# Optimization experiments

Hardware: AMD Instinct MI355X
Metric: run time of the kernel (lower is better)

## Reference

```python
import math
import jax, jax.numpy as jnp
import numpy as np

HEADS = 9
EMBED = 32
TEMPERATURE = 3000.0

def _conv1x1(x, W, b):
    # x: [B,C,H,W], W: [O,C], b: [O]  (1x1 conv == channel matmul)
    return jnp.einsum('bchw,oc->bohw', x, W) + b[None, :, None, None]

def setup_inputs() -> dict:
    key = jax.random.key(0)
    ks = jax.random.split(key, 14)
    B, H, W = 2, 64, 64
    h2, w2 = 32, 32
    hd = HEADS * EMBED  # 288
    s = 0.1
    return {
        'second_frame': jax.random.normal(ks[0], (B, 3, H, W), jnp.float32),
        'first_frame_aligned': jax.random.normal(ks[1], (B, 3, H, W), jnp.float32),
        'second_frame_feat': jax.random.normal(ks[2], (B, 4, h2, w2), jnp.float32),
        'first_frame_feat_aligned': jax.random.normal(ks[3], (B, 4, h2, w2), jnp.float32),
        'Wq': jax.random.normal(ks[4], (hd, 3), jnp.float32) * s,
        'bq': jax.random.normal(ks[5], (hd,), jnp.float32) * s,
        'Wk': jax.random.normal(ks[6], (hd, 3), jnp.float32) * s,
        'bk': jax.random.normal(ks[7], (hd,), jnp.float32) * s,
        'Wv': jax.random.normal(ks[8], (hd, 4), jnp.float32) * s,
        'bv': jax.random.normal(ks[9], (hd,), jnp.float32) * s,
        'Wp': jax.random.normal(ks[10], (4, hd), jnp.float32) * s,
        'bp': jax.random.normal(ks[11], (4,), jnp.float32) * s,
        'Wt': jax.random.normal(ks[12], (1, EMBED), jnp.float32) * s,
        'bt': jax.random.normal(ks[13], (1,), jnp.float32) * s,
    }

def reference(second_frame, first_frame_aligned, second_frame_feat,
              first_frame_feat_aligned, Wq, bq, Wk, bk, Wv, bv, Wp, bp, Wt, bt):
    B, _, H, W = second_frame.shape
    HW = H * W
    # bilinear upsample of aligned features to (H, W); half-pixel centers == align_corners=False
    feat_up = jax.image.resize(first_frame_feat_aligned,
                               (B, first_frame_feat_aligned.shape[1], H, W),
                               method='linear', antialias=False)
    Q = _conv1x1(second_frame, Wq, bq).reshape(B, HEADS, EMBED, HW)
    K = _conv1x1(first_frame_aligned, Wk, bk).reshape(B, HEADS, EMBED, HW)
    V = _conv1x1(feat_up, Wv, bv).reshape(B, HEADS, EMBED, HW)
    Qn = jnp.transpose(Q, (0, 1, 3, 2))                      # [B,h,HW,d]
    sim = jnp.einsum('bhnd,bhdm->bhnm', Qn, K) / math.sqrt(EMBED)  # [B,h,HW,HW]
    # learned per-query threshold from Q
    t = jnp.einsum('bhnd,od->bhno', Qn, Wt) + bt             # [B,h,HW,1]
    attn = jax.nn.relu((sim - t) / TEMPERATURE)              # no row normalization
    out = jnp.einsum('bhnm,bhdm->bhnd', attn, V)             # [B,h,HW,d]
    out = jnp.transpose(out, (0, 1, 3, 2)).reshape(B, HEADS * EMBED, H, W)
    out_feat = _conv1x1(out, Wp, bp)                         # [B,4,H,W]
    h2, w2 = second_frame_feat.shape[-2:]
    out_feat_down = jax.image.resize(out_feat, (B, out_feat.shape[1], h2, w2),
                                     method='linear', antialias=False)
    final_feat = second_frame_feat + out_feat_down
    return final_feat, out_feat_down
```

## Files before the change

### kernel.cpp

```cpp
#include <hip/hip_runtime.h>
#include <hip/hip_bf16.h>
#include <cstddef>

#define NHEADS 9
#define D 32
#define SQ 4096
#define ZSPLIT 8
#define MBLK (SQ / ZSPLIT)
#define CHUNKS (MBLK / 64)
#define KROW 40
#define VROW 72

typedef __attribute__((ext_vector_type(8))) short bf16x8;
typedef __attribute__((ext_vector_type(4))) short bf16x4;
typedef __attribute__((ext_vector_type(4))) float f32x4;

__device__ __forceinline__ unsigned int f2bf(float f) {
    unsigned int u = __float_as_uint(f);
    u += 0x7fffu + ((u >> 16) & 1u);
    return u >> 16;
}

__device__ __forceinline__ unsigned int trunc_pk(float lo, float hi) {
    return __builtin_amdgcn_perm(__float_as_uint(hi), __float_as_uint(lo),
                                 0x07060302u);
}

__device__ __forceinline__ bf16x8 relu_pack8(f32x4 s1, f32x4 s2) {
    const f32x4 zz = {0.f, 0.f, 0.f, 0.f};
    f32x4 a = __builtin_elementwise_max(s1, zz);
    f32x4 b = __builtin_elementwise_max(s2, zz);
    union { unsigned int u[4]; bf16x8 v; } P;
    P.u[0] = trunc_pk(a[0], a[1]);
    P.u[1] = trunc_pk(a[2], a[3]);
    P.u[2] = trunc_pk(b[0], b[1]);
    P.u[3] = trunc_pk(b[2], b[3]);
    return P.v;
}

__global__ __launch_bounds__(256) void prep_kernel(
    const float* __restrict__ x2, const float* __restrict__ x1,
    const float* __restrict__ feat1,
    const float* __restrict__ Wq, const float* __restrict__ bq,
    const float* __restrict__ Wk, const float* __restrict__ bk,
    const float* __restrict__ Wv, const float* __restrict__ bv,
    const float* __restrict__ Wt, const float* __restrict__ bt,
    unsigned short* __restrict__ Qb, unsigned short* __restrict__ Kb,
    unsigned short* __restrict__ Vt, float* __restrict__ tbuf,
    float* __restrict__ of)
{
    int idx = blockIdx.x * blockDim.x + threadIdx.x;
    if (idx < 2 * 4 * SQ) of[idx] = 0.0f;
    int g  = idx & 3;
    int n  = (idx >> 2) & (SQ - 1);
    int bh = idx >> 14;
    int h  = bh % NHEADS;
    int b  = bh / NHEADS;

    float xs0 = x2[((size_t)b * 3 + 0) * SQ + n];
    float xs1 = x2[((size_t)b * 3 + 1) * SQ + n];
    float xs2 = x2[((size_t)b * 3 + 2) * SQ + n];
    float ys0 = x1[((size_t)b * 3 + 0) * SQ + n];
    float ys1 = x1[((size_t)b * 3 + 1) * SQ + n];
    float ys2 = x1[((size_t)b * 3 + 2) * SQ + n];

    int yy = n >> 6, xx = n & 63;
    int jy = yy >> 1, jx = xx >> 1;
    int j0, j1, i0, i1; float wy0, wy1, wx0, wx1;
    if (yy & 1) { j0 = jy; j1 = (jy < 31) ? jy + 1 : 31; wy0 = 0.75f; wy1 = 0.25f; }
    else        { j0 = (jy > 0) ? jy - 1 : 0; j1 = jy;   wy0 = 0.25f; wy1 = 0.75f; }
    if (xx & 1) { i0 = jx; i1 = (jx < 31) ? jx + 1 : 31; wx0 = 0.75f; wx1 = 0.25f; }
    else        { i0 = (jx > 0) ? jx - 1 : 0; i1 = jx;   wx0 = 0.25f; wx1 = 0.75f; }

    float fu[4];
#pragma unroll
    for (int c = 0; c < 4; ++c) {
        const float* f = feat1 + ((size_t)b * 4 + c) * 1024;
        fu[c] = wy0 * (wx0 * f[j0 * 32 + i0] + wx1 * f[j0 * 32 + i1]) +
                wy1 * (wx0 * f[j1 * 32 + i0] + wx1 * f[j1 * 32 + i1]);
    }

    const int d0 = g * 8;
    unsigned int qp[4], kp[4];
    float tpart = 0.0f;
#pragma unroll
    for (int j = 0; j < 8; ++j) {
        int d = d0 + j, hd = h * D + d;
        float q = bq[hd] + Wq[hd * 3] * xs0 + Wq[hd * 3 + 1] * xs1 + Wq[hd * 3 + 2] * xs2;
        float k = bk[hd] + Wk[hd * 3] * ys0 + Wk[hd * 3 + 1] * ys1 + Wk[hd * 3 + 2] * ys2;
        float v = bv[hd] + Wv[hd * 4] * fu[0] + Wv[hd * 4 + 1] * fu[1] +
                  Wv[hd * 4 + 2] * fu[2] + Wv[hd * 4 + 3] * fu[3];
        tpart += q * Wt[d];
        unsigned int qb_ = f2bf(q), kb_ = f2bf(k);
        if (j & 1) { qp[j >> 1] |= qb_ << 16; kp[j >> 1] |= kb_ << 16; }
        else       { qp[j >> 1]  = qb_;       kp[j >> 1]  = kb_; }
        Vt[((size_t)bh * D + d) * SQ + n] = (unsigned short)f2bf(v);
    }
    tpart += __shfl_xor(tpart, 1);
    tpart += __shfl_xor(tpart, 2);
    if (g == 0) tbuf[(size_t)bh * SQ + n] = tpart + bt[0];

    size_t base = ((size_t)bh * SQ + n) * D + d0;
    *(uint4*)(Qb + base) = make_uint4(qp[0], qp[1], qp[2], qp[3]);
    *(uint4*)(Kb + base) = make_uint4(kp[0], kp[1], kp[2], kp[3]);
}

__global__ __launch_bounds__(256, 4) void attn_kernel(
    const unsigned short* __restrict__ Qb,
    const unsigned short* __restrict__ Kb,
    const unsigned short* __restrict__ Vt,
    const float* __restrict__ tbuf,
    const float* __restrict__ Wp,
    float* __restrict__ of)
{
    __shared__ __align__(16) unsigned short Ks[64 * KROW];
    __shared__ __align__(16) unsigned short Vs[32 * VROW];

    const int bh   = blockIdx.y;
    const int h    = bh % NHEADS;
    const int b    = bh / NHEADS;
    const int n0   = blockIdx.x * 256;
    const int mc0  = blockIdx.z * MBLK;
    const int tid  = threadIdx.x;
    const int wave = tid >> 6;
    const int lane = tid & 63;
    const int l15  = lane & 15;
    const int quad = lane >> 4;

    const int nw = n0 + wave * 64;

    const unsigned short* qbase = Qb + ((size_t)bh * SQ + nw + l15) * D + quad * 8;
    bf16x8 qfA = *(const bf16x8*)(qbase);
    bf16x8 qfB = *(const bf16x8*)(qbase + 16 * D);
    bf16x8 qfC = *(const bf16x8*)(qbase + 32 * D);
    bf16x8 qfD = *(const bf16x8*)(qbase + 48 * D);

    const float SQRT32 = 5.656854249492381f;
    const float* tb = tbuf + (size_t)bh * SQ + nw + l15;
    float TA = tb[0]  * SQRT32;
    float TB = tb[16] * SQRT32;
    float TC = tb[32] * SQRT32;
    float TD = tb[48] * SQRT32;
    const f32x4 ciA = {-TA, -TA, -TA, -TA};
    const f32x4 ciB = {-TB, -TB, -TB, -TB};
    const f32x4 ciC = {-TC, -TC, -TC, -TC};
    const f32x4 ciD = {-TD, -TD, -TD, -TD};

    const uint4* Kg4 = (const uint4*)(Kb + (size_t)bh * SQ * D);
    const uint4* Vg4 = (const uint4*)(Vt + (size_t)bh * D * SQ);

    const int krow = tid >> 2;
    const int kcol = (tid & 3) * 8;
    const int kslot = (krow & 32) + 4 * ((krow >> 3) & 3) + (krow & 3) + ((krow & 4) << 2);
    unsigned short* kdst = Ks + kslot * KROW + kcol;
    const int vd = tid >> 3;
    const int vm = (tid & 7) * 8;
    unsigned short* vdst = Vs + vd * VROW + vm;
    const int vgbase = vd * (SQ / 8) + (mc0 >> 3) + (tid & 7);

    f32x4 accAl = {0.f,0.f,0.f,0.f}, accAh = {0.f,0.f,0.f,0.f};
    f32x4 accBl = {0.f,0.f,0.f,0.f}, accBh = {0.f,0.f,0.f,0.f};
    f32x4 accCl = {0.f,0.f,0.f,0.f}, accCh = {0.f,0.f,0.f,0.f};
    f32x4 accDl = {0.f,0.f,0.f,0.f}, accDh = {0.f,0.f,0.f,0.f};

    uint4 kreg = Kg4[(size_t)mc0 * 4 + tid];
    uint4 vreg = Vg4[vgbase];

    for (int c = 0; c < CHUNKS; ++c) {
        __syncthreads();
        *(uint4*)kdst = kreg;
        *(uint4*)vdst = vreg;
        kreg = Kg4[(size_t)(mc0 + (c + 1) * 64) * 4 + tid];
        vreg = Vg4[vgbase + (c + 1) * 8];
        __syncthreads();

#pragma unroll
        for (int g32 = 0; g32 < 2; ++g32) {
            const unsigned short* kbase = Ks + g32 * 32 * KROW;
            bf16x8 kf1 = *(const bf16x8*)(kbase + l15 * KROW + quad * 8);
            bf16x8 kf2 = *(const bf16x8*)(kbase + (16 + l15) * KROW + quad * 8);
            bf16x8 vlo = *(const bf16x8*)(Vs + l15 * VROW + g32 * 32 + quad * 8);
            bf16x8 vhi = *(const bf16x8*)(Vs + (l15 + 16) * VROW + g32 * 32 + quad * 8);

            f32x4 sA1 = __builtin_amdgcn_mfma_f32_16x16x32_bf16(kf1, qfA, ciA, 0, 0, 0);
            f32x4 sA2 = __builtin_amdgcn_mfma_f32_16x16x32_bf16(kf2, qfA, ciA, 0, 0, 0);
            f32x4 sB1 = __builtin_amdgcn_mfma_f32_16x16x32_bf16(kf1, qfB, ciB, 0, 0, 0);
            f32x4 sB2 = __builtin_amdgcn_mfma_f32_16x16x32_bf16(kf2, qfB, ciB, 0, 0, 0);
            f32x4 sC1 = __builtin_amdgcn_mfma_f32_16x16x32_bf16(kf1, qfC, ciC, 0, 0, 0);
            f32x4 sC2 = __builtin_amdgcn_mfma_f32_16x16x32_bf16(kf2, qfC, ciC, 0, 0, 0);
            f32x4 sD1 = __builtin_amdgcn_mfma_f32_16x16x32_bf16(kf1, qfD, ciD, 0, 0, 0);
            f32x4 sD2 = __builtin_amdgcn_mfma_f32_16x16x32_bf16(kf2, qfD, ciD, 0, 0, 0);

            bf16x8 pA = relu_pack8(sA1, sA2);
            bf16x8 pB = relu_pack8(sB1, sB2);
            bf16x8 pC = relu_pack8(sC1, sC2);
            bf16x8 pD = relu_pack8(sD1, sD2);

            accAl = __builtin_amdgcn_mfma_f32_16x16x32_bf16(vlo, pA, accAl, 0, 0, 0);
            accAh = __builtin_amdgcn_mfma_f32_16x16x32_bf16(vhi, pA, accAh, 0, 0, 0);
            accBl = __builtin_amdgcn_mfma_f32_16x16x32_bf16(vlo, pB, accBl, 0, 0, 0);
            accBh = __builtin_amdgcn_mfma_f32_16x16x32_bf16(vhi, pB, accBh, 0, 0, 0);
            accCl = __builtin_amdgcn_mfma_f32_16x16x32_bf16(vlo, pC, accCl, 0, 0, 0);
            accCh = __builtin_amdgcn_mfma_f32_16x16x32_bf16(vhi, pC, accCh, 0, 0, 0);
            accDl = __builtin_amdgcn_mfma_f32_16x16x32_bf16(vlo, pD, accDl, 0, 0, 0);
            accDh = __builtin_amdgcn_mfma_f32_16x16x32_bf16(vhi, pD, accDh, 0, 0, 0);
        }
    }

    const float s1 = 5.892556509887896e-05f;
    const float* wph = Wp + h * D + quad * 4;
#pragma unroll
    for (int o = 0; o < 4; ++o) {
        float cA = 0.f, cB = 0.f, cC = 0.f, cD = 0.f;
#pragma unroll
        for (int r = 0; r < 4; ++r) {
            float wlo = wph[o * 288 + r], whi = wph[o * 288 + 16 + r];
            cA += accAl[r] * wlo + accAh[r] * whi;
            cB += accBl[r] * wlo + accBh[r] * whi;
            cC += accCl[r] * wlo + accCh[r] * whi;
            cD += accDl[r] * wlo + accDh[r] * whi;
        }
        cA += __shfl_xor(cA, 16); cA += __shfl_xor(cA, 32);
        cB += __shfl_xor(cB, 16); cB += __shfl_xor(cB, 32);
        cC += __shfl_xor(cC, 16); cC += __shfl_xor(cC, 32);
        cD += __shfl_xor(cD, 16); cD += __shfl_xor(cD, 32);
        if (quad == 0) {
            float* ob = &of[((size_t)b * 4 + o) * SQ + nw + l15];
            atomicAdd(ob,      cA * s1);
            atomicAdd(ob + 16, cB * s1);
            atomicAdd(ob + 32, cC * s1);
            atomicAdd(ob + 48, cD * s1);
        }
    }
}

__global__ void final_kernel(const float* __restrict__ of,
                             const float* __restrict__ sff,
                             const float* __restrict__ bp,
                             float* __restrict__ dout)
{
    int tid = blockIdx.x * blockDim.x + threadIdx.x;
    if (tid >= 8192) return;
    int i  = tid & 31;
    int jj = (tid >> 5) & 31;
    int bo = tid >> 10;
    int o  = bo & 3;
    const float* src = of + (size_t)bo * SQ;
    int y = jj * 2, x = i * 2;
    float dval = 0.25f * (src[y * 64 + x] + src[y * 64 + x + 1] +
                          src[(y + 1) * 64 + x] + src[(y + 1) * 64 + x + 1]) + bp[o];
    dout[tid]        = sff[tid] + dval;
    dout[8192 + tid] = dval;
}

extern "C" void kernel_launch(void* const* d_in, const int* in_sizes, int n_in,
                              void* d_out, int out_size, void* d_ws, size_t ws_size,
                              hipStream_t stream)
{
    const float* second_frame = (const float*)d_in[0];
    const float* first_frame  = (const float*)d_in[1];
    const float* sff          = (const float*)d_in[2];
    const float* ffa          = (const float*)d_in[3];
    const float* Wq = (const float*)d_in[4];
    const float* bq = (const float*)d_in[5];
    const float* Wk = (const float*)d_in[6];
    const float* bk = (const float*)d_in[7];
    const float* Wv = (const float*)d_in[8];
    const float* bv = (const float*)d_in[9];
    const float* Wp = (const float*)d_in[10];
    const float* bp = (const float*)d_in[11];
    const float* Wt = (const float*)d_in[12];
    const float* bt = (const float*)d_in[13];
    float* out = (float*)d_out;

    char* ws = (char*)d_ws;
    const size_t QKV = (size_t)2 * NHEADS * SQ * D * sizeof(unsigned short);
    unsigned short* Qb = (unsigned short*)ws;
    unsigned short* Kb = (unsigned short*)(ws + QKV);
    unsigned short* Vt = (unsigned short*)(ws + 2 * QKV);
    float* tbuf = (float*)(ws + 3 * QKV);
    float* of   = (float*)(ws + 3 * QKV + (size_t)2 * NHEADS * SQ * sizeof(float));

    prep_kernel<<<1152, 256, 0, stream>>>(second_frame, first_frame, ffa,
                                          Wq, bq, Wk, bk, Wv, bv, Wt, bt,
                                          Qb, Kb, Vt, tbuf, of);
    dim3 ag(16, 18, ZSPLIT);
    attn_kernel<<<ag, 256, 0, stream>>>(Qb, Kb, Vt, tbuf, Wp, of);
    final_kernel<<<32, 256, 0, stream>>>(of, sff, bp, out);
}
```

Baseline: 138.2 us.

## Double-buffer K/V in LDS and coalesce V transpose store via shared memory

The attention loop now uses two LDS buffers for K and V, storing the next chunk while computing the current one. This halves the barriers per chunk and uses a custom barrier that waits only on LDS counters, not on outstanding global loads. The prep kernel stages V through shared memory so the transposed V writes become coalesced 8-byte stores instead of scattered 2-byte stores. The cost is more LDS per block, which may reduce occupancy, and the prefetch loads read past the block's chunk range on the last iterations.

```diff
diff --git a/kernel.cpp b/kernel.cpp
--- a/kernel.cpp
+++ b/kernel.cpp
@@ -19,6 +19,10 @@
     unsigned int u = __float_as_uint(f);
     u += 0x7fffu + ((u >> 16) & 1u);
     return u >> 16;
+}
+
+__device__ __forceinline__ void lds_barrier() {
+    asm volatile("s_waitcnt lgkmcnt(0)\n\ts_barrier" ::: "memory");
 }
 
 __device__ __forceinline__ unsigned int trunc_pk(float lo, float hi) {
@@ -49,9 +53,13 @@
     unsigned short* __restrict__ Vt, float* __restrict__ tbuf,
     float* __restrict__ of)
 {
-    int idx = blockIdx.x * blockDim.x + threadIdx.x;
+    __shared__ unsigned short Vls[32 * 66];
+
+    const int tid = threadIdx.x;
+    int idx = blockIdx.x * blockDim.x + tid;
     if (idx < 2 * 4 * SQ) of[idx] = 0.0f;
     int g  = idx & 3;
+    int nl = tid >> 2;
     int n  = (idx >> 2) & (SQ - 1);
     int bh = idx >> 14;
     int h  = bh % NHEADS;
@@ -94,7 +102,7 @@
         unsigned int qb_ = f2bf(q), kb_ = f2bf(k);
         if (j & 1) { qp[j >> 1] |= qb_ << 16; kp[j >> 1] |= kb_ << 16; }
         else       { qp[j >> 1]  = qb_;       kp[j >> 1]  = kb_; }
-        Vt[((size_t)bh * D + d) * SQ + n] = (unsigned short)f2bf(v);
+        Vls[d * 66 + nl] = (unsigned short)f2bf(v);
     }
     tpart += __shfl_xor(tpart, 1);
     tpart += __shfl_xor(tpart, 2);
@@ -103,7 +111,49 @@
     size_t base = ((size_t)bh * SQ + n) * D + d0;
     *(uint4*)(Qb + base) = make_uint4(qp[0], qp[1], qp[2], qp[3]);
     *(uint4*)(Kb + base) = make_uint4(kp[0], kp[1], kp[2], kp[3]);
-}
+
+    __syncthreads();
+    {
+        int r  = tid >> 3;
+        int c4 = tid & 7;
+        int n0 = (blockIdx.x & 63) * 64;
+        unsigned int w0 = *(const unsigned int*)&Vls[r * 66 + c4 * 4];
+        unsigned int w1 = *(const unsigned int*)&Vls[r * 66 + c4 * 4 + 2];
+        *(uint2*)(Vt + ((size_t)bh * D + r) * SQ + n0 + c4 * 4) = make_uint2(w0, w1);
+    }
+}
+
+#define COMPUTE(KS, VS)                                                          \
+    {                                                                            \
+        _Pragma("unroll")                                                        \
+        for (int g32 = 0; g32 < 2; ++g32) {                                      \
+            const unsigned short* kbase = KS + g32 * 32 * KROW;                  \
+            bf16x8 kf1 = *(const bf16x8*)(kbase + l15 * KROW + quad * 8);        \
+            bf16x8 kf2 = *(const bf16x8*)(kbase + (16 + l15) * KROW + quad * 8); \
+            bf16x8 vlo = *(const bf16x8*)(VS + l15 * VROW + g32 * 32 + quad * 8);\
+            bf16x8 vhi = *(const bf16x8*)(VS + (l15 + 16) * VROW + g32 * 32 + quad * 8);\
+            f32x4 sA1 = __builtin_amdgcn_mfma_f32_16x16x32_bf16(kf1, qfA, ciA, 0, 0, 0);\
+            f32x4 sA2 = __builtin_amdgcn_mfma_f32_16x16x32_bf16(kf2, qfA, ciA, 0, 0, 0);\
+            f32x4 sB1 = __builtin_amdgcn_mfma_f32_16x16x32_bf16(kf1, qfB, ciB, 0, 0, 0);\
+            f32x4 sB2 = __builtin_amdgcn_mfma_f32_16x16x32_bf16(kf2, qfB, ciB, 0, 0, 0);\
+            f32x4 sC1 = __builtin_amdgcn_mfma_f32_16x16x32_bf16(kf1, qfC, ciC, 0, 0, 0);\
+            f32x4 sC2 = __builtin_amdgcn_mfma_f32_16x16x32_bf16(kf2, qfC, ciC, 0, 0, 0);\
+            f32x4 sD1 = __builtin_amdgcn_mfma_f32_16x16x32_bf16(kf1, qfD, ciD, 0, 0, 0);\
+            f32x4 sD2 = __builtin_amdgcn_mfma_f32_16x16x32_bf16(kf2, qfD, ciD, 0, 0, 0);\
+            bf16x8 pA = relu_pack8(sA1, sA2);                                    \
+            bf16x8 pB = relu_pack8(sB1, sB2);                                    \
+            bf16x8 pC = relu_pack8(sC1, sC2);                                    \
+            bf16x8 pD = relu_pack8(sD1, sD2);                                    \
+            accAl = __builtin_amdgcn_mfma_f32_16x16x32_bf16(vlo, pA, accAl, 0, 0, 0);\
+            accAh = __builtin_amdgcn_mfma_f32_16x16x32_bf16(vhi, pA, accAh, 0, 0, 0);\
+            accBl = __builtin_amdgcn_mfma_f32_16x16x32_bf16(vlo, pB, accBl, 0, 0, 0);\
+            accBh = __builtin_amdgcn_mfma_f32_16x16x32_bf16(vhi, pB, accBh, 0, 0, 0);\
+            accCl = __builtin_amdgcn_mfma_f32_16x16x32_bf16(vlo, pC, accCl, 0, 0, 0);\
+            accCh = __builtin_amdgcn_mfma_f32_16x16x32_bf16(vhi, pC, accCh, 0, 0, 0);\
+            accDl = __builtin_amdgcn_mfma_f32_16x16x32_bf16(vlo, pD, accDl, 0, 0, 0);\
+            accDh = __builtin_amdgcn_mfma_f32_16x16x32_bf16(vhi, pD, accDh, 0, 0, 0);\
+        }                                                                        \
+    }
 
 __global__ __launch_bounds__(256, 4) void attn_kernel(
     const unsigned short* __restrict__ Qb,
@@ -113,8 +163,10 @@
     const float* __restrict__ Wp,
     float* __restrict__ of)
 {
-    __shared__ __align__(16) unsigned short Ks[64 * KROW];
-    __shared__ __align__(16) unsigned short Vs[32 * VROW];
+    __shared__ __align__(16) unsigned short Ks0[64 * KROW];
+    __shared__ __align__(16) unsigned short Ks1[64 * KROW];
+    __shared__ __align__(16) unsigned short Vs0[32 * VROW];
+    __shared__ __align__(16) unsigned short Vs1[32 * VROW];
 
     const int bh   = blockIdx.y;
     const int h    = bh % NHEADS;
@@ -152,10 +204,12 @@
     const int krow = tid >> 2;
     const int kcol = (tid & 3) * 8;
     const int kslot = (krow & 32) + 4 * ((krow >> 3) & 3) + (krow & 3) + ((krow & 4) << 2);
-    unsigned short* kdst = Ks + kslot * KROW + kcol;
+    unsigned short* kdst0 = Ks0 + kslot * KROW + kcol;
+    unsigned short* kdst1 = Ks1 + kslot * KROW + kcol;
     const int vd = tid >> 3;
     const int vm = (tid & 7) * 8;
-    unsigned short* vdst = Vs + vd * VROW + vm;
+    unsigned short* vdst0 = Vs0 + vd * VROW + vm;
+    unsigned short* vdst1 = Vs1 + vd * VROW + vm;
     const int vgbase = vd * (SQ / 8) + (mc0 >> 3) + (tid & 7);
 
     f32x4 accAl = {0.f,0.f,0.f,0.f}, accAh = {0.f,0.f,0.f,0.f};
@@ -163,48 +217,27 @@
     f32x4 accCl = {0.f,0.f,0.f,0.f}, accCh = {0.f,0.f,0.f,0.f};
     f32x4 accDl = {0.f,0.f,0.f,0.f}, accDh = {0.f,0.f,0.f,0.f};
 
-    uint4 kreg = Kg4[(size_t)mc0 * 4 + tid];
-    uint4 vreg = Vg4[vgbase];
-
-    for (int c = 0; c < CHUNKS; ++c) {
-        __syncthreads();
-        *(uint4*)kdst = kreg;
-        *(uint4*)vdst = vreg;
-        kreg = Kg4[(size_t)(mc0 + (c + 1) * 64) * 4 + tid];
-        vreg = Vg4[vgbase + (c + 1) * 8];
-        __syncthreads();
-
-#pragma unroll
-        for (int g32 = 0; g32 < 2; ++g32) {
-            const unsigned short* kbase = Ks + g32 * 32 * KROW;
-            bf16x8 kf1 = *(const bf16x8*)(kbase + l15 * KROW + quad * 8);
-            bf16x8 kf2 = *(const bf16x8*)(kbase + (16 + l15) * KROW + quad * 8);
-            bf16x8 vlo = *(const bf16x8*)(Vs + l15 * VROW + g32 * 32 + quad * 8);
-            bf16x8 vhi = *(const bf16x8*)(Vs + (l15 + 16) * VROW + g32 * 32 + quad * 8);
-
-            f32x4 sA1 = __builtin_amdgcn_mfma_f32_16x16x32_bf16(kf1, qfA, ciA, 0, 0, 0);
-            f32x4 sA2 = __builtin_amdgcn_mfma_f32_16x16x32_bf16(kf2, qfA, ciA, 0, 0, 0);
-            f32x4 sB1 = __builtin_amdgcn_mfma_f32_16x16x32_bf16(kf1, qfB, ciB, 0, 0, 0);
-            f32x4 sB2 = __builtin_amdgcn_mfma_f32_16x16x32_bf16(kf2, qfB, ciB, 0, 0, 0);
-            f32x4 sC1 = __builtin_amdgcn_mfma_f32_16x16x32_bf16(kf1, qfC, ciC, 0, 0, 0);
-            f32x4 sC2 = __builtin_amdgcn_mfma_f32_16x16x32_bf16(kf2, qfC, ciC, 0, 0, 0);
-            f32x4 sD1 = __builtin_amdgcn_mfma_f32_16x16x32_bf16(kf1, qfD, ciD, 0, 0, 0);
-            f32x4 sD2 = __builtin_amdgcn_mfma_f32_16x16x32_bf16(kf2, qfD, ciD, 0, 0, 0);
-
-            bf16x8 pA = relu_pack8(sA1, sA2);
-            bf16x8 pB = relu_pack8(sB1, sB2);
-            bf16x8 pC = relu_pack8(sC1, sC2);
-            bf16x8 pD = relu_pack8(sD1, sD2);
-
-            accAl = __builtin_amdgcn_mfma_f32_16x16x32_bf16(vlo, pA, accAl, 0, 0, 0);
-            accAh = __builtin_amdgcn_mfma_f32_16x16x32_bf16(vhi, pA, accAh, 0, 0, 0);
-            accBl = __builtin_amdgcn_mfma_f32_16x16x32_bf16(vlo, pB, accBl, 0, 0, 0);
-            accBh = __builtin_amdgcn_mfma_f32_16x16x32_bf16(vhi, pB, accBh, 0, 0, 0);
-            accCl = __builtin_amdgcn_mfma_f32_16x16x32_bf16(vlo, pC, accCl, 0, 0, 0);
-            accCh = __builtin_amdgcn_mfma_f32_16x16x32_bf16(vhi, pC, accCh, 0, 0, 0);
-            accDl = __builtin_amdgcn_mfma_f32_16x16x32_bf16(vlo, pD, accDl, 0, 0, 0);
-            accDh = __builtin_amdgcn_mfma_f32_16x16x32_bf16(vhi, pD, accDh, 0, 0, 0);
-        }
+    uint4 k0 = Kg4[(size_t)mc0 * 4 + tid];
+    uint4 v0 = Vg4[vgbase];
+    *(uint4*)kdst0 = k0;
+    *(uint4*)vdst0 = v0;
+    uint4 k1 = Kg4[(size_t)(mc0 + 64) * 4 + tid];
+    uint4 v1 = Vg4[vgbase + 8];
+    lds_barrier();
+
+    for (int c = 0; c < CHUNKS; c += 2) {
+        *(uint4*)kdst1 = k1;
+        *(uint4*)vdst1 = v1;
+        k0 = Kg4[(size_t)(mc0 + (c + 2) * 64) * 4 + tid];
+        v0 = Vg4[vgbase + (c + 2) * 8];
+        COMPUTE(Ks0, Vs0);
+        lds_barrier();
+        *(uint4*)kdst0 = k0;
+        *(uint4*)vdst0 = v0;
+        k1 = Kg4[(size_t)(mc0 + (c + 3) * 64) * 4 + tid];
+        v1 = Vg4[vgbase + (c + 3) * 8];
+        COMPUTE(Ks1, Vs1);
+        lds_barrier();
     }
 
     const float s1 = 5.892556509887896e-05f;
```

Result: no change. 136.3 us (-1.4%).
